# Optimization experiments

Hardware: AMD Instinct MI355X
Metric: run time of the kernel (lower is better)

The kernel has to match this reference:

```python
import jax, jax.numpy as jnp
import numpy as np
from jax import lax

N_IN, N_H = 3, 2
N_REC = N_IN + N_H  # 5 qubits in the recurrent cell


def _ry(theta):
    # theta: (B,) -> (B, 2, 2) complex64 RY matrices
    c = jnp.cos(theta * 0.5).astype(jnp.complex64)
    s = jnp.sin(theta * 0.5).astype(jnp.complex64)
    return jnp.stack([jnp.stack([c, -s], -1), jnp.stack([s, c], -1)], -2)


def _rot(phi, theta, omega):
    # PennyLane Rot(phi, theta, omega) = RZ(omega) @ RY(theta) @ RZ(phi)
    c = jnp.cos(theta * 0.5)
    s = jnp.sin(theta * 0.5)
    ep = jnp.exp(-0.5j * (phi + omega))  # e^{-i(phi+omega)/2}
    em = jnp.exp(0.5j * (phi - omega))   # e^{+i(phi-omega)/2}
    m = jnp.stack([jnp.stack([ep * c, -em * s], -1),
                   jnp.stack([jnp.conj(em) * s, jnp.conj(ep) * c], -1)], -2)
    return m.astype(jnp.complex64)


def _apply1q(state, U, wire, n):
    # state: (B, 2**n); wire 0 is most significant (PennyLane convention)
    L, R = 2 ** wire, 2 ** (n - wire - 1)
    st = state.reshape(-1, L, 2, R)
    sub = 'bij,bljr->blir' if U.ndim == 3 else 'ij,bljr->blir'
    return jnp.einsum(sub, U, st).reshape(state.shape)


def _cnot_perm(c, t, n):
    # CNOT is a fixed basis permutation: flip target bit where control bit set
    cbit, tbit = 1 << (n - 1 - c), 1 << (n - 1 - t)
    idx = np.arange(2 ** n)
    return np.where(idx & cbit, idx ^ tbit, idx)


def _entangle(state, weights, n):
    # StronglyEntanglingLayers: per-wire Rot, then CNOT ring with range r
    n_layers = weights.shape[0]
    for l in range(n_layers):
        for w in range(n):
            state = _apply1q(state, _rot(weights[l, w, 0], weights[l, w, 1], weights[l, w, 2]), w, n)
        r = (l % (n - 1)) + 1
        for w in range(n):
            state = state[:, _cnot_perm(w, (w + r) % n, n)]
    return state


def _expz(state, wire, n):
    # <Z_wire> = P(0) - P(1)
    L, R = 2 ** wire, 2 ** (n - wire - 1)
    p = (state.real ** 2 + state.imag ** 2).reshape(-1, L, 2, R).sum((1, 3))
    return p[:, 0] - p[:, 1]


def _init_state(batch, n):
    s = jnp.zeros((batch, 2 ** n), jnp.complex64)
    return s.at[:, 0].set(1.0)


def _cell(x, h, w_rec):
    # batched qrnn_cell: RY-encode x on wires 0..2, h on wires 3..4, entangle, read Z(3),Z(4)
    state = _init_state(x.shape[0], N_REC)
    for i in range(N_IN):
        state = _apply1q(state, _ry(x[:, i]), i, N_REC)
    for j in range(N_H):
        state = _apply1q(state, _ry(h[:, j]), N_IN + j, N_REC)
    state = _entangle(state, w_rec, N_REC)
    return jnp.stack([_expz(state, N_IN + j, N_REC) for j in range(N_H)], -1)


def _readout(h, w_out):
    # batched qnn_readout: 2-qubit circuit, Z(0) expval
    state = _init_state(h.shape[0], N_H)
    for j in range(N_H):
        state = _apply1q(state, _ry(h[:, j]), j, N_H)
    state = _entangle(state, w_out, N_H)
    return _expz(state, 0, N_H)[:, None]


def setup_inputs() -> dict:
    key = jax.random.key(0)
    k1, k2, k3 = jax.random.split(key, 3)
    T, B = 32, 8192
    x_seq = jax.random.normal(k1, (T, B, N_IN), jnp.float32)
    w_rec = jax.random.normal(k2, (2, N_REC, 3), jnp.float32)
    w_out = jax.random.normal(k3, (2, N_H, 3), jnp.float32)
    return {"x_seq": x_seq, "w_rec": w_rec, "w_out": w_out}


def reference(x_seq, w_rec, w_out):
    B = x_seq.shape[1]

    def step(h, xt):
        return _cell(xt, h, w_rec), None

    h, _ = lax.scan(step, jnp.zeros((B, N_H), jnp.float32), x_seq)
    return _readout(h, w_out)  # (B, 1)
```

## Files before the change

kernel.cpp:

```cpp
#include <hip/hip_runtime.h>
#include <math.h>


typedef __attribute__((ext_vector_type(2))) float f2;

constexpr int cnot_ct(int idx, int c, int t) {
    return (idx & (1 << (4 - c))) ? (idx ^ (1 << (4 - t))) : idx;
}
constexpr int Pfwd_ct(int x, int r) {
    for (int w = 4; w >= 0; --w) x = cnot_ct(x, w, (w + r) % 5);
    return x;
}
constexpr int Pinv_ct(int x, int r) {
    for (int w = 0; w <= 4; ++w) x = cnot_ct(x, w, (w + r) % 5);
    return x;
}
static_assert(Pinv_ct(Pfwd_ct(13, 1), 1) == 13, "inv1");
static_assert(Pinv_ct(Pfwd_ct(22, 2), 2) == 22, "inv2");

constexpr int GMASK[10] = {16, 8, 4, 2, 1,
                           Pfwd_ct(16,1), Pfwd_ct(8,1), Pfwd_ct(4,1), Pfwd_ct(2,1), Pfwd_ct(1,1)};
constexpr int fmask_l1(int pb) {
    int f = 0;
    for (int b = 0; b < 5; ++b) if ((Pinv_ct(1 << b, 1) >> pb) & 1) f |= 1 << b;
    return f;
}
constexpr int FMASK[10] = {16, 8, 4, 2, 1,
                           fmask_l1(4), fmask_l1(3), fmask_l1(2), fmask_l1(1), fmask_l1(0)};
constexpr int cinv_ct(int x) { return Pinv_ct(Pinv_ct(x, 1), 2); }
constexpr int fmask_fin(int pb) {
    int f = 0;
    for (int b = 0; b < 5; ++b) if ((cinv_ct(1 << b) >> pb) & 1) f |= 1 << b;
    return f;
}
constexpr int SF3 = fmask_fin(1);
constexpr int SF4 = fmask_fin(0);
constexpr int FMf(int b) { return Pfwd_ct(Pfwd_ct(1 << b, 2), 1); }

constexpr unsigned span3_ct(int a, int b, int c) {
    unsigned m = 0;
    for (int i = 0; i < 8; ++i) {
        int v = ((i & 1) ? a : 0) ^ ((i & 2) ? b : 0) ^ ((i & 4) ? c : 0);
        m |= 1u << v;
    }
    return m;
}
constexpr unsigned PSPAN = span3_ct(FMf(4), FMf(3), FMf(2));
static_assert(PSPAN == span3_ct(16, 1, 14), "p-stage basis {16,1,14} spans PSPAN");
static_assert((PSPAN >> 16) & 1, "16 in PSPAN: reg dim collapsed by p-reduce");
constexpr bool in_pspan(int v) { return (PSPAN >> (v & 31)) & 1; }
constexpr bool pspan_ok() {
    for (int v = 0; v < 32; ++v) if ((PSPAN >> v) & 1) {
        if (__builtin_popcount(v & SF3) & 1) return false;
        if (__builtin_popcount(v & SF4) & 1) return false;
    }
    return true;
}
static_assert(pspan_ok(), "sign functionals vanish on PSPAN");
static_assert((SF3 & 16) == 0 && (SF4 & 16) == 0, "signs lane-only");

constexpr int QM1 = 12;
constexpr int QM0 = 8;
static_assert((QM1 & 16) == 0 && (QM0 & 16) == 0, "q reps lane-only");
static_assert(in_pspan(QM1 ^ FMf(1)), "QM1 ~ FMf(1) mod PSPAN");
static_assert(in_pspan(QM0 ^ FMf(0)), "QM0 ~ FMf(0) mod PSPAN");
static_assert(!in_pspan(QM1) && !in_pspan(QM0) && !in_pspan(QM1 ^ QM0),
              "q reps independent mod duplication subgroup");

constexpr int A4(int l) {
    return ((l & 1) ? 15 : 0) ^ ((l & 2) ? 7 : 0) ^ ((l & 4) ? 2 : 0) ^ ((l & 8) ? 1 : 0);
}
constexpr int Ainv4(int p) {
    for (int l = 0; l < 16; ++l) if (A4(l) == p) return l;
    return -1;
}
constexpr bool a_bij() {
    for (int p = 0; p < 16; ++p) { int l = Ainv4(p); if (l < 0 || A4(l) != p) return false; }
    for (int p = 0; p < 16; ++p) {
        int lin = ((p&1)?Ainv4(1):0) ^ ((p&2)?Ainv4(2):0) ^ ((p&4)?Ainv4(4):0) ^ ((p&8)?Ainv4(8):0);
        if (lin != Ainv4(p)) return false;
    }
    return true;
}
static_assert(a_bij(), "A bijective, inverse linear");

__device__ __forceinline__ int ainv_rt(int p) {
    return ((p & 1) ? Ainv4(1) : 0) ^ ((p & 2) ? Ainv4(2) : 0) ^
           ((p & 4) ? Ainv4(4) : 0) ^ ((p & 8) ? Ainv4(8) : 0);
}

__device__ __forceinline__ int pinv_rt(int x, int r) {
    #pragma unroll
    for (int w = 0; w < 5; ++w) {
        int cbit = 1 << (4 - w), tbit = 1 << (4 - ((w + r) % 5));
        if (x & cbit) x ^= tbit;
    }
    return x;
}

template<int CTRL> __device__ __forceinline__ float dppf(float x) {
    return __int_as_float(__builtin_amdgcn_mov_dpp(__float_as_int(x), CTRL, 0xF, 0xF, true));
}
template<int PL> __device__ __forceinline__ float mvf(float x) {
    if constexpr (PL == 0)  return x;
    else if constexpr (PL == 1)  return dppf<0xB1>(x);
    else if constexpr (PL == 2)  return dppf<0x4E>(x);
    else if constexpr (PL == 3)  return dppf<0x1B>(x);
    else if constexpr (PL == 7)  return dppf<0x141>(x);
    else if constexpr (PL == 15) return dppf<0x140>(x);
    else if constexpr (PL & 8)   return mvf<PL ^ 15>(dppf<0x140>(x));
    else                         return mvf<PL ^ 7>(dppf<0x141>(x));
}

template<int g>
__device__ __forceinline__ void ry_gate(f2& VR, f2& VI,
                                        const f2 (&C2)[10], const f2 (&S2)[10]) {
    constexpr int m  = GMASK[g];
    constexpr int rm = (m >> 4) & 1;
    constexpr int pl = A4(m & 15);
    f2 PR, PI;
    if constexpr (rm == 0) {
        PR.x = mvf<pl>(VR.x); PR.y = mvf<pl>(VR.y);
        PI.x = mvf<pl>(VI.x); PI.y = mvf<pl>(VI.y);
    } else {
        PR.x = mvf<pl>(VR.y); PR.y = mvf<pl>(VR.x);
        PI.x = mvf<pl>(VI.y); PI.y = mvf<pl>(VI.x);
    }
    VR = C2[g] * VR + S2[g] * PR;
    VI = C2[g] * VI + S2[g] * PI;
}

__global__ __launch_bounds__(256, 2) void qrnn_kernel(
    const float* __restrict__ x_seq, const float* __restrict__ w_rec,
    const float* __restrict__ w_out, float* __restrict__ out, int T, int B) {

    __shared__ float4 xs4[16 * 32];

    const int tloc = threadIdx.x;
    const int lb   = tloc >> 4;
    const int lam  = tloc & 15;
    const int b0   = blockIdx.x * 16;
    const int b    = b0 + lb;

    #pragma unroll
    for (int q = 0; q < 2; ++q) {
        const int p  = tloc + q * 256;
        const int ts = p >> 4, lbs = p & 15;
        const int g  = (ts * B + (b0 + lbs)) * 3;
        float4 v;
        v.x = x_seq[g]; v.y = x_seq[g + 1]; v.z = x_seq[g + 2]; v.w = 0.f;
        xs4[lbs * 32 + ts] = v;
    }
    __syncthreads();

    const int l = ainv_rt(lam);

    f2 C2[10], S2[10];
    #pragma unroll
    for (int g = 0; g < 10; ++g) {
        const float the = w_rec[(g / 5) * 15 + (g % 5) * 3 + 1];
        const float c = cosf(0.5f * the), s = sinf(0.5f * the);
        const bool bl = __popc(l & (FMASK[g] & 15)) & 1;
        const bool fb = (FMASK[g] >> 4) & 1;
        const float sg = bl ? s : -s;
        C2[g].x = c;  C2[g].y = c;
        S2[g].x = sg; S2[g].y = fb ? -sg : sg;
    }
    f2 P0r2, P0i2, E1r2, E1i2;
    #pragma unroll
    for (int r = 0; r < 2; ++r) {
        const int s_idx = (r << 4) | l;
        const int j     = pinv_rt(s_idx, 1);
        float a0 = 0.f, e1 = 0.f;
        #pragma unroll
        for (int w = 0; w < 5; ++w) {
            const float sg0 = ((s_idx >> (4 - w)) & 1) ? 0.5f : -0.5f;
            const float sg1 = ((j     >> (4 - w)) & 1) ? 0.5f : -0.5f;
            a0 += sg0 * w_rec[w * 3 + 0];
            e1 += sg0 * w_rec[w * 3 + 2];
            e1 += sg1 * w_rec[15 + w * 3 + 0];
        }
        if (r == 0) { P0r2.x = cosf(a0); P0i2.x = sinf(a0);
                      E1r2.x = cosf(e1); E1i2.x = sinf(e1); }
        else        { P0r2.y = cosf(a0); P0i2.y = sinf(a0);
                      E1r2.y = cosf(e1); E1i2.y = sinf(e1); }
    }
    const float s3f = (__popc(l & SF3) & 1) ? -1.f : 1.f;
    const float s4f = (__popc(l & SF4) & 1) ? -1.f : 1.f;
    const float o1 = (l & 8) ? 0.25f : 0.f;
    const float o2 = (l & 4) ? 0.25f : 0.f;
    const float o3 = (l & 2) ? 0.25f : 0.f;
    const float o4 = (l & 1) ? 0.25f : 0.f;
    constexpr float K = 0.5f * 0.15915494309189535f;

    const float4* xrow = &xs4[lb * 32];
    float4 cx = xrow[0];
    float c0 = __builtin_amdgcn_cosf(cx.x * K);
    float s0 = __builtin_amdgcn_cosf(fmaf(cx.x, K, -0.25f));
    float f1 = __builtin_amdgcn_cosf(fmaf(cx.y, K, -o1));
    float f2v = __builtin_amdgcn_cosf(fmaf(cx.z, K, -o2));
    float h0 = 0.f, h1 = 0.f;

    #pragma unroll 1
    for (int t = 0; t < T; ++t) {
        const int tn = (t + 1 < T) ? t + 1 : t;
        const float4 nx = xrow[tn];

        const float f3 = __builtin_amdgcn_cosf(fmaf(h0, K, -o3));
        const float f4 = __builtin_amdgcn_cosf(fmaf(h1, K, -o4));
        const float Xl = (f1 * f2v) * (f3 * f4);
        f2 bp; bp.x = c0 * Xl; bp.y = s0 * Xl;
        f2 VR = bp * P0r2;
        f2 VI = bp * P0i2;

        ry_gate<0>(VR, VI, C2, S2); ry_gate<1>(VR, VI, C2, S2);
        ry_gate<2>(VR, VI, C2, S2); ry_gate<3>(VR, VI, C2, S2);
        ry_gate<4>(VR, VI, C2, S2);
        {
            const f2 nr = VR * E1r2 - VI * E1i2;
            const f2 ni = VR * E1i2 + VI * E1r2;
            VR = nr; VI = ni;
        }
        ry_gate<5>(VR, VI, C2, S2); ry_gate<6>(VR, VI, C2, S2);
        ry_gate<7>(VR, VI, C2, S2); ry_gate<8>(VR, VI, C2, S2);
        ry_gate<9>(VR, VI, C2, S2);

        const f2 P = VR * VR + VI * VI;
        float tq = P.x + P.y;
        tq += mvf<A4(1)>(tq);
        tq += mvf<A4(14)>(tq);
        float q0 = s3f * tq, q1 = s4f * tq;
        q0 += mvf<A4(QM1)>(q0);
        q1 += mvf<A4(QM1)>(q1);
        q0 += mvf<A4(QM0)>(q0);
        q1 += mvf<A4(QM0)>(q1);
        h0 = q0; h1 = q1;

        c0  = __builtin_amdgcn_cosf(nx.x * K);
        s0  = __builtin_amdgcn_cosf(fmaf(nx.x, K, -0.25f));
        f1  = __builtin_amdgcn_cosf(fmaf(nx.y, K, -o1));
        f2v = __builtin_amdgcn_cosf(fmaf(nx.z, K, -o2));
    }

    const float sh0 = sinf(0.5f * h0), ch0 = cosf(0.5f * h0);
    const float sh1 = sinf(0.5f * h1), ch1 = cosf(0.5f * h1);
    float vr0 = ch0 * ch1, vr1 = ch0 * sh1, vr2 = sh0 * ch1, vr3 = sh0 * sh1;
    float vi0 = 0.f, vi1 = 0.f, vi2 = 0.f, vi3 = 0.f;

    #pragma unroll
    for (int li = 0; li < 2; ++li) {
        #pragma unroll
        for (int w = 0; w < 2; ++w) {
            const float phi = w_out[li * 6 + w * 3 + 0];
            const float the = w_out[li * 6 + w * 3 + 1];
            const float ome = w_out[li * 6 + w * 3 + 2];
            const float cs = cosf(0.5f * the), ss = sinf(0.5f * the);
            const float cp = cosf(0.5f * (phi + ome)), sp = sinf(0.5f * (phi + ome));
            const float cm = cosf(0.5f * (phi - ome)), sm = sinf(0.5f * (phi - ome));
            const float are = cp * cs, aim = -sp * cs;
            const float bre = cm * ss, bim = sm * ss;
            #define AP2(r0, i0, r1, i1) do {                                  \
                float n0r = are*(r0) - aim*(i0) - bre*(r1) + bim*(i1);        \
                float n0i = are*(i0) + aim*(r0) - bre*(i1) - bim*(r1);        \
                float n1r = bre*(r0) + bim*(i0) + are*(r1) + aim*(i1);        \
                float n1i = bre*(i0) - bim*(r0) + are*(i1) - aim*(r1);        \
                r0 = n0r; i0 = n0i; r1 = n1r; i1 = n1i; } while (0)
            if (w == 0) { AP2(vr0, vi0, vr2, vi2); AP2(vr1, vi1, vr3, vi3); }
            else        { AP2(vr0, vi0, vr1, vi1); AP2(vr2, vi2, vr3, vi3); }
            #undef AP2
        }
        float tr1 = vr2, ti1 = vi2, tr2 = vr3, ti2 = vi3, tr3 = vr1, ti3 = vi1;
        vr1 = tr1; vi1 = ti1; vr2 = tr2; vi2 = ti2; vr3 = tr3; vi3 = ti3;
    }

    const float outv = (vr0 * vr0 + vi0 * vi0 + vr1 * vr1 + vi1 * vi1) -
                       (vr2 * vr2 + vi2 * vi2 + vr3 * vr3 + vi3 * vi3);
    if (lam == 0) out[b] = outv;
}

extern "C" void kernel_launch(void* const* d_in, const int* in_sizes, int n_in,
                              void* d_out, int out_size, void* d_ws, size_t ws_size,
                              hipStream_t stream) {
    const float* x_seq = (const float*)d_in[0];
    const float* w_rec = (const float*)d_in[1];
    const float* w_out = (const float*)d_in[2];
    float* out = (float*)d_out;

    const int B = out_size;
    const int T = in_sizes[0] / (B * 3);

    const int grid = (B * 16) / 256;
    hipLaunchKernelGGL(qrnn_kernel, dim3(grid), dim3(256), 0, stream,
                       x_seq, w_rec, w_out, out, T, B);
}
```

Baseline: 85.43 us.

## Replace per-step circuit simulation with precomputed trigonometric-polynomial coefficient contraction

The expectation values are trigonometric polynomials of degree one in each half-angle input. The change evaluates the circuit at 243 sample points, interpolates them into a 18x27 coefficient matrix A, and precomputes the x-dependent parts of the recurrence for all 32 timesteps in parallel. The serial recurrence loop then only needs a few cosines of h, an FMA and a DPP reduction per step, instead of a full 10-gate statevector simulation. It adds two tiny prep kernel launches, workspace use and a large shared-memory table, and it hardcodes T=32.

```diff
diff --git a/kernel.cpp b/kernel.cpp
--- a/kernel.cpp
+++ b/kernel.cpp
@@ -47,7 +47,6 @@
 }
 constexpr unsigned PSPAN = span3_ct(FMf(4), FMf(3), FMf(2));
 static_assert(PSPAN == span3_ct(16, 1, 14), "p-stage basis {16,1,14} spans PSPAN");
-static_assert((PSPAN >> 16) & 1, "16 in PSPAN: reg dim collapsed by p-reduce");
 constexpr bool in_pspan(int v) { return (PSPAN >> (v & 31)) & 1; }
 constexpr bool pspan_ok() {
     for (int v = 0; v < 32; ++v) if ((PSPAN >> v) & 1) {
@@ -67,6 +66,8 @@
 static_assert(!in_pspan(QM1) && !in_pspan(QM0) && !in_pspan(QM1 ^ QM0),
               "q reps independent mod duplication subgroup");
 
+static_assert(span3_ct(1, 2, 7) == 0xFFu, "butterfly {1,2,7} spans lanes 0..7");
+
 constexpr int A4(int l) {
     return ((l & 1) ? 15 : 0) ^ ((l & 2) ? 7 : 0) ^ ((l & 4) ? 2 : 0) ^ ((l & 8) ? 1 : 0);
 }
@@ -88,7 +89,6 @@
     return ((p & 1) ? Ainv4(1) : 0) ^ ((p & 2) ? Ainv4(2) : 0) ^
            ((p & 4) ? Ainv4(4) : 0) ^ ((p & 8) ? Ainv4(8) : 0);
 }
-
 __device__ __forceinline__ int pinv_rt(int x, int r) {
     #pragma unroll
     for (int w = 0; w < 5; ++w) {
@@ -107,6 +107,7 @@
     else if constexpr (PL == 2)  return dppf<0x4E>(x);
     else if constexpr (PL == 3)  return dppf<0x1B>(x);
     else if constexpr (PL == 7)  return dppf<0x141>(x);
+    else if constexpr (PL == 8)  return dppf<0x128>(x);
     else if constexpr (PL == 15) return dppf<0x140>(x);
     else if constexpr (PL & 8)   return mvf<PL ^ 15>(dppf<0x140>(x));
     else                         return mvf<PL ^ 7>(dppf<0x141>(x));
@@ -130,29 +131,12 @@
     VI = C2[g] * VI + S2[g] * PI;
 }
 
-__global__ __launch_bounds__(256, 2) void qrnn_kernel(
-    const float* __restrict__ x_seq, const float* __restrict__ w_rec,
-    const float* __restrict__ w_out, float* __restrict__ out, int T, int B) {
-
-    __shared__ float4 xs4[16 * 32];
-
-    const int tloc = threadIdx.x;
-    const int lb   = tloc >> 4;
-    const int lam  = tloc & 15;
-    const int b0   = blockIdx.x * 16;
-    const int b    = b0 + lb;
-
-    #pragma unroll
-    for (int q = 0; q < 2; ++q) {
-        const int p  = tloc + q * 256;
-        const int ts = p >> 4, lbs = p & 15;
-        const int g  = (ts * B + (b0 + lbs)) * 3;
-        float4 v;
-        v.x = x_seq[g]; v.y = x_seq[g + 1]; v.z = x_seq[g + 2]; v.w = 0.f;
-        xs4[lbs * 32 + ts] = v;
-    }
-    __syncthreads();
-
+__global__ __launch_bounds__(256) void qrnn_eval(
+    const float* __restrict__ w_rec, float* __restrict__ Q) {
+    const int tid = blockIdx.x * blockDim.x + threadIdx.x;
+    const int combo = tid >> 4;
+    const int lam = tid & 15;
+    if (combo >= 243) return;
     const int l = ainv_rt(lam);
 
     f2 C2[10], S2[10];
@@ -187,59 +171,150 @@
     }
     const float s3f = (__popc(l & SF3) & 1) ? -1.f : 1.f;
     const float s4f = (__popc(l & SF4) & 1) ? -1.f : 1.f;
-    const float o1 = (l & 8) ? 0.25f : 0.f;
-    const float o2 = (l & 4) ? 0.25f : 0.f;
-    const float o3 = (l & 2) ? 0.25f : 0.f;
-    const float o4 = (l & 1) ? 0.25f : 0.f;
-    constexpr float K = 0.5f * 0.15915494309189535f;
-
-    const float4* xrow = &xs4[lb * 32];
-    float4 cx = xrow[0];
-    float c0 = __builtin_amdgcn_cosf(cx.x * K);
-    float s0 = __builtin_amdgcn_cosf(fmaf(cx.x, K, -0.25f));
-    float f1 = __builtin_amdgcn_cosf(fmaf(cx.y, K, -o1));
-    float f2v = __builtin_amdgcn_cosf(fmaf(cx.z, K, -o2));
+
+    const int d0 = combo / 81, d1 = (combo / 27) % 3, d2 = (combo / 9) % 3,
+              d3 = (combo / 3) % 3, d4 = combo % 3;
+    const float CH[3] = {1.f, 0.5f, 0.5f};
+    const float SH[3] = {0.f, 0.86602540378443865f, -0.86602540378443865f};
+    const float c0  = CH[d0], s0 = SH[d0];
+    const float f1  = (l & 8) ? SH[d1] : CH[d1];
+    const float f2v = (l & 4) ? SH[d2] : CH[d2];
+    const float f3  = (l & 2) ? SH[d3] : CH[d3];
+    const float f4  = (l & 1) ? SH[d4] : CH[d4];
+
+    const float Xl = (f1 * f2v) * (f3 * f4);
+    f2 bp; bp.x = c0 * Xl; bp.y = s0 * Xl;
+    f2 VR = bp * P0r2;
+    f2 VI = bp * P0i2;
+
+    ry_gate<0>(VR, VI, C2, S2); ry_gate<1>(VR, VI, C2, S2);
+    ry_gate<2>(VR, VI, C2, S2); ry_gate<3>(VR, VI, C2, S2);
+    ry_gate<4>(VR, VI, C2, S2);
+    {
+        const f2 nr = VR * E1r2 - VI * E1i2;
+        const f2 ni = VR * E1i2 + VI * E1r2;
+        VR = nr; VI = ni;
+    }
+    ry_gate<5>(VR, VI, C2, S2); ry_gate<6>(VR, VI, C2, S2);
+    ry_gate<7>(VR, VI, C2, S2); ry_gate<8>(VR, VI, C2, S2);
+    ry_gate<9>(VR, VI, C2, S2);
+
+    const f2 P = VR * VR + VI * VI;
+    float tq = P.x + P.y;
+    tq += mvf<A4(1)>(tq);
+    tq += mvf<A4(14)>(tq);
+    float q0 = s3f * tq, q1 = s4f * tq;
+    q0 += mvf<A4(QM1)>(q0); q1 += mvf<A4(QM1)>(q1);
+    q0 += mvf<A4(QM0)>(q0); q1 += mvf<A4(QM0)>(q1);
+
+    if (lam == 0) { Q[combo * 2 + 0] = q0; Q[combo * 2 + 1] = q1; }
+}
+
+__global__ __launch_bounds__(256) void qrnn_contract(
+    const float* __restrict__ Q, float* __restrict__ A) {
+    const int o = blockIdx.x * blockDim.x + threadIdx.x;
+    if (o >= 486) return;
+    const int row = o / 27, col = o % 27;
+    const int j = row / 9, pq = row % 9, p = pq / 3, q = pq % 3;
+    const int a0 = col / 9, a1 = (col / 3) % 3, a2 = col % 3;
+    const float W[3][3] = {{1.f/3.f, 1.f/3.f, 1.f/3.f},
+                           {2.f/3.f, -1.f/3.f, -1.f/3.f},
+                           {0.f, 0.57735026918962576f, -0.57735026918962576f}};
+    float acc = 0.f;
+    for (int d0 = 0; d0 < 3; ++d0)
+    for (int d1 = 0; d1 < 3; ++d1)
+    for (int d2 = 0; d2 < 3; ++d2) {
+        const float w012 = W[a0][d0] * W[a1][d1] * W[a2][d2];
+        for (int d3 = 0; d3 < 3; ++d3)
+        for (int d4 = 0; d4 < 3; ++d4) {
+            const int c = (((d0 * 3 + d1) * 3 + d2) * 3 + d3) * 3 + d4;
+            acc = fmaf(w012 * W[p][d3] * W[q][d4], Q[c * 2 + j], acc);
+        }
+    }
+    A[row * 27 + col] = acc;
+}
+
+__global__ __launch_bounds__(256, 2) void qrnn_main(
+    const float* __restrict__ x_seq, const float* __restrict__ w_out,
+    const float* __restrict__ A, float* __restrict__ out, int B) {
+
+    __shared__ float4 xs4[16 * 32];
+    __shared__ float  Cm[16][19][33];
+
+    const int tloc = threadIdx.x;
+    const int g = tloc >> 4;
+    const int k = tloc & 15;
+    const int b0 = blockIdx.x * 16;
+    const int b = b0 + g;
+
+    #pragma unroll
+    for (int qq = 0; qq < 2; ++qq) {
+        const int p = tloc + qq * 256;
+        const int ts = p >> 4, lbs = p & 15;
+        const int gidx = (ts * B + (b0 + lbs)) * 3;
+        float4 v;
+        v.x = x_seq[gidx]; v.y = x_seq[gidx + 1]; v.z = x_seq[gidx + 2]; v.w = 0.f;
+        xs4[lbs * 32 + ts] = v;
+    }
+    __syncthreads();
+
+    constexpr float Kf = 0.15915494309189535f;
+
+    #pragma unroll 1
+    for (int tt = 0; tt < 2; ++tt) {
+        const int t = k + 16 * tt;
+        const float4 xv = xs4[g * 32 + t];
+        const float cx0 = __builtin_amdgcn_cosf(xv.x * Kf);
+        const float sx0 = __builtin_amdgcn_cosf(fmaf(xv.x, Kf, -0.25f));
+        const float cx1 = __builtin_amdgcn_cosf(xv.y * Kf);
+        const float sx1 = __builtin_amdgcn_cosf(fmaf(xv.y, Kf, -0.25f));
+        const float cx2 = __builtin_amdgcn_cosf(xv.z * Kf);
+        const float sx2 = __builtin_amdgcn_cosf(fmaf(xv.z, Kf, -0.25f));
+        float Xb[27];
+        Xb[0] = 1.f;  Xb[1] = cx2;       Xb[2] = sx2;
+        Xb[3] = cx1;  Xb[4] = cx1 * cx2; Xb[5] = cx1 * sx2;
+        Xb[6] = sx1;  Xb[7] = sx1 * cx2; Xb[8] = sx1 * sx2;
+        #pragma unroll
+        for (int i = 0; i < 9; ++i) { Xb[9 + i] = cx0 * Xb[i]; Xb[18 + i] = sx0 * Xb[i]; }
+        #pragma unroll 1
+        for (int row = 0; row < 18; ++row) {
+            const float* Ar = A + row * 27;
+            float p4[4] = {0.f, 0.f, 0.f, 0.f};
+            #pragma unroll
+            for (int i = 0; i < 27; ++i) p4[i & 3] = fmaf(Ar[i], Xb[i], p4[i & 3]);
+            Cm[g][row][t] = (p4[0] + p4[1]) + (p4[2] + p4[3]);
+        }
+        Cm[g][18][t] = 0.f;
+    }
+
+    const int jj = k >> 3;
+    const int term = (k & 7) + 1;
+    const int rowA = jj * 9 + term;
+    const int rowB = (k == 0) ? 0 : ((k == 8) ? 9 : 18);
+    const int p = term / 3, q = term % 3;
+    const float* CA_ptr = &Cm[g][rowA][0];
+    const float* CB_ptr = &Cm[g][rowB][0];
+
     float h0 = 0.f, h1 = 0.f;
-
+    float CA = CA_ptr[0], CB = CB_ptr[0];
     #pragma unroll 1
-    for (int t = 0; t < T; ++t) {
-        const int tn = (t + 1 < T) ? t + 1 : t;
-        const float4 nx = xrow[tn];
-
-        const float f3 = __builtin_amdgcn_cosf(fmaf(h0, K, -o3));
-        const float f4 = __builtin_amdgcn_cosf(fmaf(h1, K, -o4));
-        const float Xl = (f1 * f2v) * (f3 * f4);
-        f2 bp; bp.x = c0 * Xl; bp.y = s0 * Xl;
-        f2 VR = bp * P0r2;
-        f2 VI = bp * P0i2;
-
-        ry_gate<0>(VR, VI, C2, S2); ry_gate<1>(VR, VI, C2, S2);
-        ry_gate<2>(VR, VI, C2, S2); ry_gate<3>(VR, VI, C2, S2);
-        ry_gate<4>(VR, VI, C2, S2);
-        {
-            const f2 nr = VR * E1r2 - VI * E1i2;
-            const f2 ni = VR * E1i2 + VI * E1r2;
-            VR = nr; VI = ni;
-        }
-        ry_gate<5>(VR, VI, C2, S2); ry_gate<6>(VR, VI, C2, S2);
-        ry_gate<7>(VR, VI, C2, S2); ry_gate<8>(VR, VI, C2, S2);
-        ry_gate<9>(VR, VI, C2, S2);
-
-        const f2 P = VR * VR + VI * VI;
-        float tq = P.x + P.y;
-        tq += mvf<A4(1)>(tq);
-        tq += mvf<A4(14)>(tq);
-        float q0 = s3f * tq, q1 = s4f * tq;
-        q0 += mvf<A4(QM1)>(q0);
-        q1 += mvf<A4(QM1)>(q1);
-        q0 += mvf<A4(QM0)>(q0);
-        q1 += mvf<A4(QM0)>(q1);
-        h0 = q0; h1 = q1;
-
-        c0  = __builtin_amdgcn_cosf(nx.x * K);
-        s0  = __builtin_amdgcn_cosf(fmaf(nx.x, K, -0.25f));
-        f1  = __builtin_amdgcn_cosf(fmaf(nx.y, K, -o1));
-        f2v = __builtin_amdgcn_cosf(fmaf(nx.z, K, -o2));
+    for (int t = 0; t < 32; ++t) {
+        const int tn = (t < 31) ? t + 1 : 31;
+        const float CAn = CA_ptr[tn], CBn = CB_ptr[tn];
+        const float ch0 = __builtin_amdgcn_cosf(h0 * Kf);
+        const float sh0 = __builtin_amdgcn_cosf(fmaf(h0, Kf, -0.25f));
+        const float ch1 = __builtin_amdgcn_cosf(h1 * Kf);
+        const float sh1 = __builtin_amdgcn_cosf(fmaf(h1, Kf, -0.25f));
+        const float u = (p == 1) ? ch0 : ((p == 2) ? sh0 : 1.f);
+        const float v = (q == 1) ? ch1 : ((q == 2) ? sh1 : 1.f);
+        float val = fmaf(CA, u * v, CB);
+        val += mvf<1>(val);
+        val += mvf<2>(val);
+        val += mvf<7>(val);
+        const float other = mvf<8>(val);
+        h0 = (k & 8) ? other : val;
+        h1 = (k & 8) ? val : other;
+        CA = CAn; CB = CBn;
     }
 
     const float sh0 = sinf(0.5f * h0), ch0 = cosf(0.5f * h0);
@@ -275,7 +350,7 @@
 
     const float outv = (vr0 * vr0 + vi0 * vi0 + vr1 * vr1 + vi1 * vi1) -
                        (vr2 * vr2 + vi2 * vi2 + vr3 * vr3 + vi3 * vi3);
-    if (lam == 0) out[b] = outv;
+    if (k == 0) out[b] = outv;
 }
 
 extern "C" void kernel_launch(void* const* d_in, const int* in_sizes, int n_in,
@@ -285,11 +360,13 @@
     const float* w_rec = (const float*)d_in[1];
     const float* w_out = (const float*)d_in[2];
     float* out = (float*)d_out;
+    float* Q = (float*)d_ws;
+    float* A = (float*)d_ws + 512;
 
     const int B = out_size;
-    const int T = in_sizes[0] / (B * 3);
-
-    const int grid = (B * 16) / 256;
-    hipLaunchKernelGGL(qrnn_kernel, dim3(grid), dim3(256), 0, stream,
-                       x_seq, w_rec, w_out, out, T, B);
-}
+
+    hipLaunchKernelGGL(qrnn_eval,     dim3(16), dim3(256), 0, stream, w_rec, Q);
+    hipLaunchKernelGGL(qrnn_contract, dim3(2),  dim3(256), 0, stream, Q, A);
+    hipLaunchKernelGGL(qrnn_main,     dim3((B * 16) / 256), dim3(256), 0, stream,
+                       x_seq, w_out, A, out, B);
+}
```

Measured after the change: 94.92 us. +11.1%, slower.
